# Kernel tuning notes

Hardware: AMD Instinct MI355X
Metric: run time of the kernel (lower is better)

The kernel has to match this reference:

```python
import jax, jax.numpy as jnp
import numpy as np

B, S, D, H, F = 8, 1024, 1024, 16, 4096
DH = D // H  # 64
EPS = 1e-12


def _layer_norm(x, g, b):
    mu = jnp.mean(x, axis=-1, keepdims=True)
    var = jnp.mean(jnp.square(x - mu), axis=-1, keepdims=True)
    return (x - mu) / jnp.sqrt(var + EPS) * g + b


def setup_inputs() -> dict:
    key = jax.random.key(0)
    ks = jax.random.split(key, 16)
    sd = 0.02
    inp = {
        "x": jax.random.normal(ks[0], (B, S, D), dtype=jnp.float32),
        "attn_mask": jnp.ones((B, S), dtype=jnp.int32),
        # attention projections (torch Linear: W is [out, in])
        "Wq": jax.random.normal(ks[1], (D, D), dtype=jnp.float32) * sd,
        "bq": jnp.zeros((D,), dtype=jnp.float32),
        "Wk": jax.random.normal(ks[2], (D, D), dtype=jnp.float32) * sd,
        "bk": jnp.zeros((D,), dtype=jnp.float32),
        "Wv": jax.random.normal(ks[3], (D, D), dtype=jnp.float32) * sd,
        "bv": jnp.zeros((D,), dtype=jnp.float32),
        "Wo": jax.random.normal(ks[4], (D, D), dtype=jnp.float32) * sd,
        "bo": jnp.zeros((D,), dtype=jnp.float32),
        # sa_layer_norm
        "ln1_g": jnp.ones((D,), dtype=jnp.float32),
        "ln1_b": jnp.zeros((D,), dtype=jnp.float32),
        # FFN
        "W1": jax.random.normal(ks[5], (F, D), dtype=jnp.float32) * sd,
        "b1": jnp.zeros((F,), dtype=jnp.float32),
        "W2": jax.random.normal(ks[6], (D, F), dtype=jnp.float32) * sd,
        "b2": jnp.zeros((D,), dtype=jnp.float32),
        # output_layer_norm
        "ln2_g": jnp.ones((D,), dtype=jnp.float32),
        "ln2_b": jnp.zeros((D,), dtype=jnp.float32),
    }
    return inp


def reference(x, attn_mask, Wq, bq, Wk, bk, Wv, bv, Wo, bo,
              ln1_g, ln1_b, W1, b1, W2, b2, ln2_g, ln2_b):
    b, s, d = x.shape

    def proj_heads(inp, W, bias):
        y = jnp.einsum('bsd,ed->bse', inp, W) + bias  # torch Linear: x @ W.T + b
        return y.reshape(b, s, H, DH).transpose(0, 2, 1, 3)  # (b, h, s, dh)

    q = proj_heads(x, Wq, bq) / jnp.sqrt(jnp.float32(DH))
    k = proj_heads(x, Wk, bk)
    v = proj_heads(x, Wv, bv)

    scores = jnp.einsum('bhqe,bhke->bhqk', q, k)  # (b, h, s, s)
    pad = (attn_mask == 0)[:, None, None, :]      # (b, 1, 1, s)
    scores = jnp.where(pad, -jnp.inf, scores)
    weights = jax.nn.softmax(scores, axis=-1)

    ctx = jnp.einsum('bhqk,bhke->bhqe', weights, v)
    ctx = ctx.transpose(0, 2, 1, 3).reshape(b, s, d)
    sa_out = jnp.einsum('bsd,ed->bse', ctx, Wo) + bo

    h = _layer_norm(sa_out + x, ln1_g, ln1_b)

    ff = jnp.einsum('bsd,fd->bsf', h, W1) + b1
    ff = jax.nn.gelu(ff, approximate=False)
    ff = jnp.einsum('bsf,df->bsd', ff, W2) + b2

    out = _layer_norm(ff + h, ln2_g, ln2_b)
    return out
```

## Files before the change

kernel.cpp:

```cpp
#include <hip/hip_runtime.h>
#include <math.h>

typedef __attribute__((ext_vector_type(8))) short short8;
typedef __attribute__((ext_vector_type(4))) float f32x4;

__device__ __forceinline__ unsigned short f2bf(float f) {
  unsigned int u = __float_as_uint(f);
  u += 0x7fffu + ((u >> 16) & 1u);
  return (unsigned short)(u >> 16);
}

__device__ __forceinline__ float gelu_f(float v) {
  float xa = fabsf(v) * 0.70710678118f;
  float t = __builtin_amdgcn_rcpf(1.f + 0.3275911f * xa);
  float p = t * (0.254829592f +
            t * (-0.284496736f +
            t * (1.421413741f +
            t * (-1.453152027f + t * 1.061405429f))));
  float erfa = 1.f - p * __expf(-xa * xa);
  return 0.5f * v * (1.f + copysignf(erfa, v));
}

__device__ __forceinline__ void gll16(const unsigned short* g, unsigned short* l) {
  __builtin_amdgcn_global_load_lds(
      (const __attribute__((address_space(1))) unsigned int*)(uintptr_t)g,
      (__attribute__((address_space(3))) unsigned int*)(uintptr_t)l, 16, 0, 0);
}

__global__ __launch_bounds__(256) void cvt_f32_bf16(const float* __restrict__ in,
                                                    unsigned short* __restrict__ out,
                                                    int n4) {
  int i = blockIdx.x * 256 + threadIdx.x;
  if (i >= n4) return;
  float4 f = reinterpret_cast<const float4*>(in)[i];
  ushort4 o;
  o.x = f2bf(f.x); o.y = f2bf(f.y); o.z = f2bf(f.z); o.w = f2bf(f.w);
  reinterpret_cast<ushort4*>(out)[i] = o;
}

__global__ __launch_bounds__(256) void cvt4_f32_bf16(
    const float* __restrict__ a, const float* __restrict__ b,
    const float* __restrict__ c, const float* __restrict__ d,
    unsigned short* __restrict__ oa, unsigned short* __restrict__ ob,
    unsigned short* __restrict__ oc, unsigned short* __restrict__ od) {
  const float* in = (blockIdx.y == 0) ? a : (blockIdx.y == 1) ? b : (blockIdx.y == 2) ? c : d;
  unsigned short* out = (blockIdx.y == 0) ? oa : (blockIdx.y == 1) ? ob : (blockIdx.y == 2) ? oc : od;
  int i = blockIdx.x * 256 + threadIdx.x;
  float4 f = reinterpret_cast<const float4*>(in)[i];
  ushort4 o;
  o.x = f2bf(f.x); o.y = f2bf(f.y); o.z = f2bf(f.z); o.w = f2bf(f.w);
  reinterpret_cast<ushort4*>(out)[i] = o;
}

template <int EPI, bool SWAP>
__global__ __launch_bounds__(256) void gemm_nt(
    const unsigned short* __restrict__ A, const unsigned short* __restrict__ B,
    const float* __restrict__ bias, const float* __restrict__ bias_k,
    int K, int N, const float* __restrict__ resid,
    unsigned short* __restrict__ outb, float* __restrict__ outf) {
  __shared__ __align__(16) unsigned short As[128 * 32];
  __shared__ __align__(16) unsigned short Bs[128 * 32];
  const int t = threadIdx.x;
  const int lin = blockIdx.x + gridDim.x * blockIdx.y;
  const int rem = lin & (gridDim.x * 8 - 1);
  const int mt = (lin / (gridDim.x * 8)) * 8 + (rem & 7);
  const int tm = mt * 128, tn = (rem >> 3) * 128;
  const int lane = t & 63, wv = t >> 6;
  const int wr = wv >> 1, wc = wv & 1;
  const int l15 = lane & 15, quad = lane >> 4;
  const int srow = lane >> 2;
  const int scol = (lane & 3) << 3;

  const unsigned short* pa0 = &A[(size_t)(tm + (wv * 2) * 16 + srow) * K + scol];
  const unsigned short* pa1 = &A[(size_t)(tm + (wv * 2 + 1) * 16 + srow) * K + scol];
  const unsigned short* pb0 = &B[(size_t)(tn + (wv * 2) * 16 + srow) * K + scol];
  const unsigned short* pb1 = &B[(size_t)(tn + (wv * 2 + 1) * 16 + srow) * K + scol];
  unsigned short* la0 = &As[(wv * 2) * 512];
  unsigned short* la1 = &As[(wv * 2 + 1) * 512];
  unsigned short* lb0 = &Bs[(wv * 2) * 512];
  unsigned short* lb1 = &Bs[(wv * 2 + 1) * 512];

  const f32x4 zero = {0.f, 0.f, 0.f, 0.f};
  f32x4 acc[4][4];
#pragma unroll
  for (int i = 0; i < 4; ++i)
#pragma unroll
    for (int j = 0; j < 4; ++j) acc[i][j] = zero;

  for (int k0 = 0; k0 < K; k0 += 32) {
    __syncthreads();
    gll16(pa0, la0); pa0 += 32;
    gll16(pa1, la1); pa1 += 32;
    gll16(pb0, lb0); pb0 += 32;
    gll16(pb1, lb1); pb1 += 32;
    __syncthreads();
    short8 af[4], bfr[4];
#pragma unroll
    for (int i = 0; i < 4; ++i) {
      af[i] = *reinterpret_cast<const short8*>(&As[(wr * 64 + i * 16 + l15) * 32 + quad * 8]);
      bfr[i] = *reinterpret_cast<const short8*>(&Bs[(wc * 64 + i * 16 + l15) * 32 + quad * 8]);
    }
#pragma unroll
    for (int i = 0; i < 4; ++i)
#pragma unroll
      for (int j = 0; j < 4; ++j)
        acc[i][j] = SWAP
            ? __builtin_amdgcn_mfma_f32_16x16x32_bf16(bfr[j], af[i], acc[i][j], 0, 0, 0)
            : __builtin_amdgcn_mfma_f32_16x16x32_bf16(af[i], bfr[j], acc[i][j], 0, 0, 0);
  }

  if (SWAP) {
#pragma unroll
    for (int i = 0; i < 4; ++i) {
      const int row = tm + wr * 64 + i * 16 + l15;
#pragma unroll
      for (int j = 0; j < 4; ++j) {
        const int col0 = tn + wc * 64 + j * 16 + quad * 4;
        if (EPI == 5) {
          const int chunk = col0 >> 10;
          const int colc = col0 & 1023;
          const float4 b4 = *reinterpret_cast<const float4*>(
              &(chunk == 0 ? bias : bias_k)[colc]);
          const float sc = (chunk == 0) ? 0.125f : 1.f;
          const int h = colc >> 6, dh = colc & 63;
          const int b = row >> 10, s = row & 1023;
          ushort4 pk;
          pk.x = f2bf((acc[i][j][0] + b4.x) * sc);
          pk.y = f2bf((acc[i][j][1] + b4.y) * sc);
          pk.z = f2bf((acc[i][j][2] + b4.z) * sc);
          pk.w = f2bf((acc[i][j][3] + b4.w) * sc);
          *reinterpret_cast<ushort4*>(
              &outb[((size_t)chunk << 23) + (((size_t)((b << 4) + h)) << 16) + (s << 6) + dh]) = pk;
        } else if (EPI == 2) {
          const float4 b4 = *reinterpret_cast<const float4*>(&bias[col0]);
          ushort4 pk;
          pk.x = f2bf(gelu_f(acc[i][j][0] + b4.x));
          pk.y = f2bf(gelu_f(acc[i][j][1] + b4.y));
          pk.z = f2bf(gelu_f(acc[i][j][2] + b4.z));
          pk.w = f2bf(gelu_f(acc[i][j][3] + b4.w));
          *reinterpret_cast<ushort4*>(&outb[(size_t)row * (size_t)N + col0]) = pk;
        } else {
          const float4 b4 = *reinterpret_cast<const float4*>(&bias[col0]);
          const size_t idx = (size_t)row * (size_t)N + col0;
          const float4 r4 = *reinterpret_cast<const float4*>(&resid[idx]);
          float4 o4;
          o4.x = acc[i][j][0] + b4.x + r4.x;
          o4.y = acc[i][j][1] + b4.y + r4.y;
          o4.z = acc[i][j][2] + b4.z + r4.z;
          o4.w = acc[i][j][3] + b4.w + r4.w;
          *reinterpret_cast<float4*>(&outf[idx]) = o4;
        }
      }
    }
  } else {
#pragma unroll
    for (int i = 0; i < 4; ++i) {
#pragma unroll
      for (int j = 0; j < 4; ++j) {
        const int col = tn + wc * 64 + j * 16 + l15;
        const float bcol = bias[col];
        const int h = col >> 6, dh = col & 63;
        const int row0 = tm + wr * 64 + i * 16 + quad * 4;
        const int b = row0 >> 10, s0 = row0 & 1023;
        ushort4 pk;
        pk.x = f2bf(acc[i][j][0] + bcol);
        pk.y = f2bf(acc[i][j][1] + bcol);
        pk.z = f2bf(acc[i][j][2] + bcol);
        pk.w = f2bf(acc[i][j][3] + bcol);
        *reinterpret_cast<ushort4*>(
            &outb[(((size_t)((b << 4) + h)) << 16) + (dh << 10) + s0]) = pk;
      }
    }
  }
}

__global__ __launch_bounds__(256) void attn_kernel(
    const unsigned short* __restrict__ Q, const unsigned short* __restrict__ Kc,
    const unsigned short* __restrict__ Vg, const int* __restrict__ mask,
    unsigned short* __restrict__ ctx) {
  __shared__ __align__(16) unsigned short Qs[64 * 64];
  __shared__ __align__(16) unsigned short Ks[64 * 64];
  __shared__ __align__(16) unsigned short Vs[64 * 64];
  __shared__ __align__(16) unsigned short Ps[4 * 16 * 72];
  __shared__ float maskf[1024];
  const int t = threadIdx.x;
  const int bh = blockIdx.x;
  const int qt = blockIdx.y;
  const int b = bh >> 4, h = bh & 15;
  const int lane = t & 63, wv = t >> 6, l15 = lane & 15, quad = lane >> 4;
  const int lr = lane >> 3;
  const int cs = (lane & 7) ^ lr;
  const unsigned short* Qp = Q + ((size_t)bh << 16);
  const unsigned short* Kp = Kc + ((size_t)bh << 16);
  const unsigned short* Vp = Vg + ((size_t)bh << 16);

  for (int i = t; i < 1024; i += 256)
    maskf[i] = mask[b * 1024 + i] ? -8.f : -INFINITY;
#pragma unroll
  for (int i = 0; i < 2; ++i) {
    const int seg = wv * 2 + i;
    gll16(&Qp[(qt * 64 + seg * 8 + lr) * 64 + cs * 8], &Qs[seg * 512]);
  }
  __syncthreads();
  const int sw0 = ((quad ^ (l15 & 7)) << 3);
  const int sw1 = (((quad + 4) ^ (l15 & 7)) << 3);
  const short8 qf0 = *reinterpret_cast<const short8*>(&Qs[(wv * 16 + l15) * 64 + sw0]);
  const short8 qf1 = *reinterpret_cast<const short8*>(&Qs[(wv * 16 + l15) * 64 + sw1]);

  const f32x4 zero = {0.f, 0.f, 0.f, 0.f};
  float ps[4] = {0.f, 0.f, 0.f, 0.f};
  f32x4 o[4];
#pragma unroll
  for (int j = 0; j < 4; ++j) o[j] = zero;

  unsigned short* Pw = &Ps[wv * 16 * 72];
  for (int kt = 0; kt < 16; ++kt) {
    __syncthreads();
#pragma unroll
    for (int i = 0; i < 2; ++i) {
      const int seg = wv * 2 + i;
      const int row = seg * 8 + lr;
      gll16(&Kp[(kt * 64 + row) * 64 + cs * 8], &Ks[seg * 512]);
      gll16(&Vp[row * 1024 + kt * 64 + cs * 8], &Vs[seg * 512]);
    }
    __syncthreads();

    f32x4 s4[4];
    float madd[4];
#pragma unroll
    for (int nt = 0; nt < 4; ++nt) {
      const int row = nt * 16 + l15;
      short8 kf0 = *reinterpret_cast<const short8*>(&Ks[row * 64 + sw0]);
      short8 kf1 = *reinterpret_cast<const short8*>(&Ks[row * 64 + sw1]);
      s4[nt] = __builtin_amdgcn_mfma_f32_16x16x32_bf16(qf0, kf0, zero, 0, 0, 0);
      s4[nt] = __builtin_amdgcn_mfma_f32_16x16x32_bf16(qf1, kf1, s4[nt], 0, 0, 0);
      madd[nt] = maskf[kt * 64 + nt * 16 + l15];
    }
#pragma unroll
    for (int nt = 0; nt < 4; ++nt) {
#pragma unroll
      for (int r = 0; r < 4; ++r) {
        float p = __expf(s4[nt][r] + madd[nt]);
        ps[r] += p;
        Pw[(quad * 4 + r) * 72 + nt * 16 + l15] = f2bf(p);
      }
    }
    short8 pf0 = *reinterpret_cast<const short8*>(&Pw[l15 * 72 + quad * 8]);
    short8 pf1 = *reinterpret_cast<const short8*>(&Pw[l15 * 72 + 32 + quad * 8]);
#pragma unroll
    for (int nt = 0; nt < 4; ++nt) {
      const int row = nt * 16 + l15;
      short8 vf0 = *reinterpret_cast<const short8*>(&Vs[row * 64 + sw0]);
      short8 vf1 = *reinterpret_cast<const short8*>(&Vs[row * 64 + sw1]);
      o[nt] = __builtin_amdgcn_mfma_f32_16x16x32_bf16(pf0, vf0, o[nt], 0, 0, 0);
      o[nt] = __builtin_amdgcn_mfma_f32_16x16x32_bf16(pf1, vf1, o[nt], 0, 0, 0);
    }
  }

#pragma unroll
  for (int r = 0; r < 4; ++r) {
#pragma unroll
    for (int off = 8; off >= 1; off >>= 1) ps[r] += __shfl_xor(ps[r], off, 64);
  }
#pragma unroll
  for (int r = 0; r < 4; ++r) {
    float inv = 1.f / ps[r];
    int srow = qt * 64 + wv * 16 + quad * 4 + r;
#pragma unroll
    for (int nt = 0; nt < 4; ++nt) {
      int dh = nt * 16 + l15;
      ctx[((size_t)b << 20) + ((size_t)srow << 10) + (h << 6) + dh] = f2bf(o[nt][r] * inv);
    }
  }
}

__global__ __launch_bounds__(256) void ln_kernel(float* __restrict__ y,
                                                 const float* __restrict__ g,
                                                 const float* __restrict__ be,
                                                 unsigned short* __restrict__ hb) {
  __shared__ float sm[8];
  const int t = threadIdx.x;
  const size_t row = blockIdx.x;
  float* yr = y + (row << 10);
  float v[4];
#pragma unroll
  for (int i = 0; i < 4; ++i) v[i] = yr[t + (i << 8)];
  float s = v[0] + v[1] + v[2] + v[3];
#pragma unroll
  for (int off = 32; off >= 1; off >>= 1) s += __shfl_xor(s, off, 64);
  if ((t & 63) == 0) sm[t >> 6] = s;
  __syncthreads();
  float mu = (sm[0] + sm[1] + sm[2] + sm[3]) * (1.f / 1024.f);
  float q = 0.f;
#pragma unroll
  for (int i = 0; i < 4; ++i) { float d = v[i] - mu; q += d * d; }
#pragma unroll
  for (int off = 32; off >= 1; off >>= 1) q += __shfl_xor(q, off, 64);
  if ((t & 63) == 0) sm[4 + (t >> 6)] = q;
  __syncthreads();
  float var = (sm[4] + sm[5] + sm[6] + sm[7]) * (1.f / 1024.f);
  float rs = rsqrtf(var + 1e-12f);
#pragma unroll
  for (int i = 0; i < 4; ++i) {
    int c = t + (i << 8);
    float o = (v[i] - mu) * rs * g[c] + be[c];
    yr[c] = o;
    if (hb) hb[(row << 10) + c] = f2bf(o);
  }
}

extern "C" void kernel_launch(void* const* d_in, const int* in_sizes, int n_in,
                              void* d_out, int out_size, void* d_ws, size_t ws_size,
                              hipStream_t stream) {
  const float* x   = (const float*)d_in[0];
  const int*   msk = (const int*)d_in[1];
  const float* Wq  = (const float*)d_in[2];
  const float* bq  = (const float*)d_in[3];
  const float* Wk  = (const float*)d_in[4];
  const float* bk  = (const float*)d_in[5];
  const float* Wv  = (const float*)d_in[6];
  const float* bv  = (const float*)d_in[7];
  const float* Wo  = (const float*)d_in[8];
  const float* bo  = (const float*)d_in[9];
  const float* g1  = (const float*)d_in[10];
  const float* be1 = (const float*)d_in[11];
  const float* W1  = (const float*)d_in[12];
  const float* b1  = (const float*)d_in[13];
  const float* W2  = (const float*)d_in[14];
  const float* b2  = (const float*)d_in[15];
  const float* g2  = (const float*)d_in[16];
  const float* be2 = (const float*)d_in[17];
  float* out = (float*)d_out;

  unsigned short* Wqb = (unsigned short*)d_ws;
  unsigned short* Wkb = Wqb + (1u << 20);
  unsigned short* Wvb = Wkb + (1u << 20);
  unsigned short* Wob = Wvb + (1u << 20);
  unsigned short* W1b = Wob + (1u << 20);
  unsigned short* W2b = W1b + (4u << 20);
  unsigned short* xb  = W2b + (4u << 20);
  unsigned short* qb  = xb + (8u << 20);
  unsigned short* vb  = qb + (16u << 20);
  unsigned short* ctx = xb;
  unsigned short* ffb = xb;
  float* y1 = (float*)(qb + (24u << 20));
  unsigned short* hb = (unsigned short*)(y1 + (8u << 20));

  dim3 blk(256);
  cvt4_f32_bf16<<<dim3(1024, 4), blk, 0, stream>>>(Wq, Wk, Wv, Wo, Wqb, Wkb, Wvb, Wob);
  cvt_f32_bf16<<<dim3(4096), blk, 0, stream>>>(W1, W1b, 1 << 20);
  cvt_f32_bf16<<<dim3(4096), blk, 0, stream>>>(W2, W2b, 1 << 20);
  cvt_f32_bf16<<<dim3(8192), blk, 0, stream>>>(x, xb, 1 << 21);
  gemm_nt<5, true><<<dim3(16, 64), blk, 0, stream>>>(xb, Wqb, bq, bk, 1024, 1024,
                                                     nullptr, qb, nullptr);
  gemm_nt<4, false><<<dim3(8, 64), blk, 0, stream>>>(xb, Wvb, bv, nullptr, 1024, 1024,
                                                     nullptr, vb, nullptr);
  attn_kernel<<<dim3(128, 16), blk, 0, stream>>>(qb, qb + (8u << 20), vb, msk, ctx);
  gemm_nt<1, true><<<dim3(8, 64), blk, 0, stream>>>(ctx, Wob, bo, nullptr, 1024, 1024,
                                                    x, nullptr, y1);
  ln_kernel<<<dim3(8192), blk, 0, stream>>>(y1, g1, be1, hb);
  gemm_nt<2, true><<<dim3(32, 64), blk, 0, stream>>>(hb, W1b, b1, nullptr, 1024, 4096,
                                                     nullptr, ffb, nullptr);
  gemm_nt<1, true><<<dim3(8, 64), blk, 0, stream>>>(ffb, W2b, b2, nullptr, 4096, 1024,
                                                    y1, nullptr, out);
  ln_kernel<<<dim3(8192), blk, 0, stream>>>(out, g2, be2, nullptr);
}
```

Measured before the change: 590.8 us.

## Double-buffer LDS tiles in GEMM and attention to overlap loads with MFMA

The GEMM and attention kernels now keep two shared-memory buffers per operand. The next K-slice (or K/V tile) is issued with global_load_lds before computing on the current one, and only one barrier runs per iteration instead of two. The goal is to hide global-load latency behind MFMA work and cut barrier stalls, at the cost of twice the LDS per block, which may lower occupancy. The GEMM also drops its grouped tile rasterization and uses a plain blockIdx mapping, which can hurt L2 reuse.

```diff
diff --git a/kernel.cpp b/kernel.cpp
--- a/kernel.cpp
+++ b/kernel.cpp
@@ -58,27 +58,24 @@
     const float* __restrict__ bias, const float* __restrict__ bias_k,
     int K, int N, const float* __restrict__ resid,
     unsigned short* __restrict__ outb, float* __restrict__ outf) {
-  __shared__ __align__(16) unsigned short As[128 * 32];
-  __shared__ __align__(16) unsigned short Bs[128 * 32];
+  __shared__ __align__(16) unsigned short As[2][128 * 32];
+  __shared__ __align__(16) unsigned short Bs[2][128 * 32];
   const int t = threadIdx.x;
-  const int lin = blockIdx.x + gridDim.x * blockIdx.y;
-  const int rem = lin & (gridDim.x * 8 - 1);
-  const int mt = (lin / (gridDim.x * 8)) * 8 + (rem & 7);
-  const int tm = mt * 128, tn = (rem >> 3) * 128;
+  const int tm = blockIdx.y * 128, tn = blockIdx.x * 128;
   const int lane = t & 63, wv = t >> 6;
   const int wr = wv >> 1, wc = wv & 1;
   const int l15 = lane & 15, quad = lane >> 4;
   const int srow = lane >> 2;
   const int scol = (lane & 3) << 3;
 
-  const unsigned short* pa0 = &A[(size_t)(tm + (wv * 2) * 16 + srow) * K + scol];
-  const unsigned short* pa1 = &A[(size_t)(tm + (wv * 2 + 1) * 16 + srow) * K + scol];
-  const unsigned short* pb0 = &B[(size_t)(tn + (wv * 2) * 16 + srow) * K + scol];
-  const unsigned short* pb1 = &B[(size_t)(tn + (wv * 2 + 1) * 16 + srow) * K + scol];
-  unsigned short* la0 = &As[(wv * 2) * 512];
-  unsigned short* la1 = &As[(wv * 2 + 1) * 512];
-  unsigned short* lb0 = &Bs[(wv * 2) * 512];
-  unsigned short* lb1 = &Bs[(wv * 2 + 1) * 512];
+  const unsigned short* pa0 = &A[(size_t)(tm + wv * 32 + srow) * K + scol];
+  const unsigned short* pa1 = &A[(size_t)(tm + wv * 32 + 16 + srow) * K + scol];
+  const unsigned short* pb0 = &B[(size_t)(tn + wv * 32 + srow) * K + scol];
+  const unsigned short* pb1 = &B[(size_t)(tn + wv * 32 + 16 + srow) * K + scol];
+  unsigned short* la0 = &As[0][(wv * 2) * 512];
+  unsigned short* la1 = &As[0][(wv * 2 + 1) * 512];
+  unsigned short* lb0 = &Bs[0][(wv * 2) * 512];
+  unsigned short* lb1 = &Bs[0][(wv * 2 + 1) * 512];
 
   const f32x4 zero = {0.f, 0.f, 0.f, 0.f};
   f32x4 acc[4][4];
@@ -87,18 +84,27 @@
 #pragma unroll
     for (int j = 0; j < 4; ++j) acc[i][j] = zero;
 
-  for (int k0 = 0; k0 < K; k0 += 32) {
+  gll16(pa0, la0); pa0 += 32;
+  gll16(pa1, la1); pa1 += 32;
+  gll16(pb0, lb0); pb0 += 32;
+  gll16(pb1, lb1); pb1 += 32;
+
+  const int nIter = K >> 5;
+  for (int it = 0; it < nIter; ++it) {
     __syncthreads();
-    gll16(pa0, la0); pa0 += 32;
-    gll16(pa1, la1); pa1 += 32;
-    gll16(pb0, lb0); pb0 += 32;
-    gll16(pb1, lb1); pb1 += 32;
-    __syncthreads();
+    const int cur = (it & 1) * 4096;
+    const int nxt = 4096 - cur;
+    if (it + 1 < nIter) {
+      gll16(pa0, la0 + nxt); pa0 += 32;
+      gll16(pa1, la1 + nxt); pa1 += 32;
+      gll16(pb0, lb0 + nxt); pb0 += 32;
+      gll16(pb1, lb1 + nxt); pb1 += 32;
+    }
     short8 af[4], bfr[4];
 #pragma unroll
     for (int i = 0; i < 4; ++i) {
-      af[i] = *reinterpret_cast<const short8*>(&As[(wr * 64 + i * 16 + l15) * 32 + quad * 8]);
-      bfr[i] = *reinterpret_cast<const short8*>(&Bs[(wc * 64 + i * 16 + l15) * 32 + quad * 8]);
+      af[i] = *reinterpret_cast<const short8*>(&As[0][cur + (wr * 64 + i * 16 + l15) * 32 + quad * 8]);
+      bfr[i] = *reinterpret_cast<const short8*>(&Bs[0][cur + (wc * 64 + i * 16 + l15) * 32 + quad * 8]);
     }
 #pragma unroll
     for (int i = 0; i < 4; ++i)
@@ -179,8 +185,8 @@
     const unsigned short* __restrict__ Vg, const int* __restrict__ mask,
     unsigned short* __restrict__ ctx) {
   __shared__ __align__(16) unsigned short Qs[64 * 64];
-  __shared__ __align__(16) unsigned short Ks[64 * 64];
-  __shared__ __align__(16) unsigned short Vs[64 * 64];
+  __shared__ __align__(16) unsigned short Ks[2][64 * 64];
+  __shared__ __align__(16) unsigned short Vs[2][64 * 64];
   __shared__ __align__(16) unsigned short Ps[4 * 16 * 72];
   __shared__ float maskf[1024];
   const int t = threadIdx.x;
@@ -193,6 +199,8 @@
   const unsigned short* Qp = Q + ((size_t)bh << 16);
   const unsigned short* Kp = Kc + ((size_t)bh << 16);
   const unsigned short* Vp = Vg + ((size_t)bh << 16);
+  const int seg0 = wv * 2, seg1 = wv * 2 + 1;
+  const int r0 = seg0 * 8 + lr, r1 = seg1 * 8 + lr;
 
   for (int i = t; i < 1024; i += 256)
     maskf[i] = mask[b * 1024 + i] ? -8.f : -INFINITY;
@@ -201,6 +209,10 @@
     const int seg = wv * 2 + i;
     gll16(&Qp[(qt * 64 + seg * 8 + lr) * 64 + cs * 8], &Qs[seg * 512]);
   }
+  gll16(&Kp[r0 * 64 + cs * 8], &Ks[0][seg0 * 512]);
+  gll16(&Kp[r1 * 64 + cs * 8], &Ks[0][seg1 * 512]);
+  gll16(&Vp[r0 * 1024 + cs * 8], &Vs[0][seg0 * 512]);
+  gll16(&Vp[r1 * 1024 + cs * 8], &Vs[0][seg1 * 512]);
   __syncthreads();
   const int sw0 = ((quad ^ (l15 & 7)) << 3);
   const int sw1 = (((quad + 4) ^ (l15 & 7)) << 3);
@@ -215,23 +227,22 @@
 
   unsigned short* Pw = &Ps[wv * 16 * 72];
   for (int kt = 0; kt < 16; ++kt) {
-    __syncthreads();
-#pragma unroll
-    for (int i = 0; i < 2; ++i) {
-      const int seg = wv * 2 + i;
-      const int row = seg * 8 + lr;
-      gll16(&Kp[(kt * 64 + row) * 64 + cs * 8], &Ks[seg * 512]);
-      gll16(&Vp[row * 1024 + kt * 64 + cs * 8], &Vs[seg * 512]);
-    }
-    __syncthreads();
+    const int cur = kt & 1;
+    if (kt < 15) {
+      const int nb = cur ^ 1;
+      gll16(&Kp[((kt + 1) * 64 + r0) * 64 + cs * 8], &Ks[nb][seg0 * 512]);
+      gll16(&Kp[((kt + 1) * 64 + r1) * 64 + cs * 8], &Ks[nb][seg1 * 512]);
+      gll16(&Vp[r0 * 1024 + (kt + 1) * 64 + cs * 8], &Vs[nb][seg0 * 512]);
+      gll16(&Vp[r1 * 1024 + (kt + 1) * 64 + cs * 8], &Vs[nb][seg1 * 512]);
+    }
 
     f32x4 s4[4];
     float madd[4];
 #pragma unroll
     for (int nt = 0; nt < 4; ++nt) {
       const int row = nt * 16 + l15;
-      short8 kf0 = *reinterpret_cast<const short8*>(&Ks[row * 64 + sw0]);
-      short8 kf1 = *reinterpret_cast<const short8*>(&Ks[row * 64 + sw1]);
+      short8 kf0 = *reinterpret_cast<const short8*>(&Ks[cur][row * 64 + sw0]);
+      short8 kf1 = *reinterpret_cast<const short8*>(&Ks[cur][row * 64 + sw1]);
       s4[nt] = __builtin_amdgcn_mfma_f32_16x16x32_bf16(qf0, kf0, zero, 0, 0, 0);
       s4[nt] = __builtin_amdgcn_mfma_f32_16x16x32_bf16(qf1, kf1, s4[nt], 0, 0, 0);
       madd[nt] = maskf[kt * 64 + nt * 16 + l15];
@@ -250,11 +261,12 @@
 #pragma unroll
     for (int nt = 0; nt < 4; ++nt) {
       const int row = nt * 16 + l15;
-      short8 vf0 = *reinterpret_cast<const short8*>(&Vs[row * 64 + sw0]);
-      short8 vf1 = *reinterpret_cast<const short8*>(&Vs[row * 64 + sw1]);
+      short8 vf0 = *reinterpret_cast<const short8*>(&Vs[cur][row * 64 + sw0]);
+      short8 vf1 = *reinterpret_cast<const short8*>(&Vs[cur][row * 64 + sw1]);
       o[nt] = __builtin_amdgcn_mfma_f32_16x16x32_bf16(pf0, vf0, o[nt], 0, 0, 0);
       o[nt] = __builtin_amdgcn_mfma_f32_16x16x32_bf16(pf1, vf1, o[nt], 0, 0, 0);
     }
+    __syncthreads();
   }
 
 #pragma unroll
```

After: 568.5 us. 1.04x faster.
